# Optimization experiments

Measured on AMD Instinct MI355X. Metric: run time of the kernel, lower is better.

Reference implementation:

```python
import jax, jax.numpy as jnp
import numpy as np

BN_EPS = 1e-3  # Keras BatchNormalization default epsilon


def setup_inputs() -> dict:
    key = jax.random.key(0)
    ks = jax.random.split(key, 8)
    N, F, H, S, E = 30000, 16, 16, 8, 300000
    return {
        "x": jax.random.normal(ks[0], (N, F), dtype=jnp.float32),
        "e": jax.random.uniform(ks[1], (E, S), dtype=jnp.float32),
        "src": jax.random.randint(ks[2], (E,), 0, N),
        "dst": jax.random.randint(ks[3], (E,), 0, N),
        "Wk": jax.random.normal(ks[4], (S, F * H), dtype=jnp.float32) * 0.1,
        "bk": jnp.zeros((F * H,), dtype=jnp.float32),
        "Wr": jax.random.normal(ks[5], (F, H), dtype=jnp.float32) * 0.1,
        "br": jnp.zeros((H,), dtype=jnp.float32),
        "gamma": jnp.ones((H,), dtype=jnp.float32),
        "beta": jnp.zeros((H,), dtype=jnp.float32),
        "mmean": jnp.zeros((H,), dtype=jnp.float32),
        "mvar": jnp.ones((H,), dtype=jnp.float32),
        "Wd": jax.random.normal(ks[6], (H, 3), dtype=jnp.float32) * 0.1,
        "bd": jnp.zeros((3,), dtype=jnp.float32),
    }


def reference(x, e, src, dst, Wk, bk, Wr, br, gamma, beta, mmean, mvar, Wd, bd):
    N, F = x.shape
    H = Wr.shape[1]
    # ECCConv: per-edge filter generated from edge features -> [E, F, H]
    kernels = (e @ Wk + bk).reshape(e.shape[0], F, H)
    # message: gather source node feats, apply per-edge kernel
    msg = jnp.einsum('ef,efh->eh', x[src], kernels)  # [E, H]
    # scatter-sum aggregate to target nodes
    agg = jax.ops.segment_sum(msg, dst, num_segments=N)  # [N, H]
    h = jax.nn.relu(agg + x @ Wr + br)
    # BatchNormalization (inference: moving stats); Dropout = identity at eval
    h = (h - mmean) / jnp.sqrt(mvar + BN_EPS) * gamma + beta
    pooled = jnp.max(h, axis=0, keepdims=True)  # GlobalMaxPool, single mode -> [1, H]
    return pooled @ Wd + bd  # [1, 3]
```

## Files before the change

### kernel.cpp

```cpp
#include <hip/hip_runtime.h>

#define BN_EPS 1e-3f

typedef float vf4 __attribute__((ext_vector_type(4)));
typedef _Float16 half8 __attribute__((ext_vector_type(8)));

__device__ __forceinline__ unsigned int f2k(float f) {
    unsigned int u = __float_as_uint(f);
    return (u & 0x80000000u) ? ~u : (u | 0x80000000u);
}
__device__ __forceinline__ float k2f(unsigned int u) {
    return __uint_as_float((u & 0x80000000u) ? (u & 0x7FFFFFFFu) : ~u);
}

template <int S, int F, int H>
__global__ void node_pre(const float* __restrict__ x,
                         const float* __restrict__ Wk,
                         const float* __restrict__ bk,
                         const float* __restrict__ Wr,
                         const float* __restrict__ br,
                         _Float16* __restrict__ y2h,
                         float* __restrict__ agg,
                         unsigned int* __restrict__ pooled_u,
                         int N) {
    if (blockIdx.x == 0 && threadIdx.x < H) pooled_u[threadIdx.x] = 0u;

    int t = blockIdx.x * blockDim.x + threadIdx.x;
    int n = t / H;
    int h = t % H;
    if (n >= N) return;

    float xf[F];
#pragma unroll
    for (int f = 0; f < F; ++f) xf[f] = x[n * F + f];

    _Float16* yrow = y2h + (size_t)n * (S + 1) * H + h;
#pragma unroll
    for (int s = 0; s < S; ++s) {
        float acc = 0.f;
#pragma unroll
        for (int f = 0; f < F; ++f) acc += xf[f] * Wk[(s * F + f) * H + h];
        yrow[s * H] = (_Float16)acc;
    }

    float accb = 0.f, accr = 0.f;
#pragma unroll
    for (int f = 0; f < F; ++f) {
        accb += xf[f] * bk[f * H + h];
        accr += xf[f] * Wr[f * H + h];
    }
    yrow[S * H] = (_Float16)accb;
    agg[(size_t)n * H + h] = accr + br[h];
}

template <int S, int H>
__global__ void __launch_bounds__(256)
edge_scatter(const float* __restrict__ efeat,
             const int* __restrict__ src,
             const int* __restrict__ dst,
             const _Float16* __restrict__ y2h,
             float* __restrict__ agg,
             int E) {
    constexpr int EB = 256;
    constexpr int LDW = EB + 4;
    __shared__ float msg[H][LDW];
    __shared__ int sdst[EB];

    int t = threadIdx.x;
    int e0 = blockIdx.x * EB;

    int el = t >> 1;
    int hi = t & 1;
    int ell0 = el, ell1 = el + 128;
    int ec0 = min(e0 + ell0, E - 1);
    int ec1 = min(e0 + ell1, E - 1);

    int sn0 = __builtin_nontemporal_load(src + ec0);
    int sn1 = __builtin_nontemporal_load(src + ec1);
    if (hi == 0) {
        sdst[ell0] = __builtin_nontemporal_load(dst + ec0);
        sdst[ell1] = __builtin_nontemporal_load(dst + ec1);
    }

    const vf4* e40 = (const vf4*)(efeat + (size_t)ec0 * S);
    const vf4* e41 = (const vf4*)(efeat + (size_t)ec1 * S);
    vf4 ea0 = __builtin_nontemporal_load(e40);
    vf4 eb0 = __builtin_nontemporal_load(e40 + 1);
    vf4 ea1 = __builtin_nontemporal_load(e41);
    vf4 eb1 = __builtin_nontemporal_load(e41 + 1);
    float es0[S + 1] = {ea0.x, ea0.y, ea0.z, ea0.w, eb0.x, eb0.y, eb0.z, eb0.w, 1.0f};
    float es1[S + 1] = {ea1.x, ea1.y, ea1.z, ea1.w, eb1.x, eb1.y, eb1.z, eb1.w, 1.0f};

    const _Float16* yb0 = y2h + (size_t)sn0 * (S + 1) * H + hi * 8;
    const _Float16* yb1 = y2h + (size_t)sn1 * (S + 1) * H + hi * 8;

    float m0[8] = {0.f, 0.f, 0.f, 0.f, 0.f, 0.f, 0.f, 0.f};
    float m1[8] = {0.f, 0.f, 0.f, 0.f, 0.f, 0.f, 0.f, 0.f};
#pragma unroll
    for (int s = 0; s <= S; ++s) {
        half8 hv0 = *(const half8*)(yb0 + s * H);
        half8 hv1 = *(const half8*)(yb1 + s * H);
#pragma unroll
        for (int j = 0; j < 8; ++j) {
            m0[j] += es0[s] * (float)hv0[j];
            m1[j] += es1[s] * (float)hv1[j];
        }
    }
#pragma unroll
    for (int j = 0; j < 8; ++j) {
        msg[hi * 8 + j][ell0] = m0[j];
        msg[hi * 8 + j][ell1] = m1[j];
    }

    __syncthreads();

    int e2 = t >> 4;
    int h = t & 15;
#pragma unroll
    for (int p = 0; p < 16; ++p) {
        int el2 = p * 16 + e2;
        if (e0 + el2 < E) {
            unsafeAtomicAdd(&agg[(size_t)sdst[el2] * H + h], msg[h][el2]);
        }
    }
}

template <int H>
__global__ void bn_relu_max(const float* __restrict__ agg,
                            const float* __restrict__ gamma,
                            const float* __restrict__ beta,
                            const float* __restrict__ mmean,
                            const float* __restrict__ mvar,
                            unsigned int* __restrict__ pooled_u,
                            int N) {
    __shared__ unsigned int smax[H];
    if (threadIdx.x < H) smax[threadIdx.x] = 0u;
    __syncthreads();

    int t = blockIdx.x * blockDim.x + threadIdx.x;
    int stride = gridDim.x * blockDim.x;
    int h = t % H;

    float scale = gamma[h] * rsqrtf(mvar[h] + BN_EPS);
    float shift = beta[h] - mmean[h] * scale;

    float best = -INFINITY;
    int total = N * H;
    for (int i = t; i < total; i += stride) {
        float v = agg[i];
        v = v > 0.f ? v : 0.f;
        v = v * scale + shift;
        best = fmaxf(best, v);
    }
    atomicMax(&smax[h], f2k(best));
    __syncthreads();
    if (threadIdx.x < H) atomicMax(&pooled_u[threadIdx.x], smax[threadIdx.x]);
}

template <int H>
__global__ void final_matvec(const unsigned int* __restrict__ pooled_u,
                             const float* __restrict__ Wd,
                             const float* __restrict__ bd,
                             float* __restrict__ out,
                             int HOUT) {
    int j = threadIdx.x;
    if (j >= HOUT) return;
    float acc = bd[j];
#pragma unroll
    for (int hh = 0; hh < H; ++hh) acc += k2f(pooled_u[hh]) * Wd[hh * HOUT + j];
    out[j] = acc;
}

extern "C" void kernel_launch(void* const* d_in, const int* in_sizes, int n_in,
                              void* d_out, int out_size, void* d_ws, size_t ws_size,
                              hipStream_t stream) {
    const float* x     = (const float*)d_in[0];
    const float* e     = (const float*)d_in[1];
    const int*   src   = (const int*)d_in[2];
    const int*   dst   = (const int*)d_in[3];
    const float* Wk    = (const float*)d_in[4];
    const float* bk    = (const float*)d_in[5];
    const float* Wr    = (const float*)d_in[6];
    const float* br    = (const float*)d_in[7];
    const float* gamma = (const float*)d_in[8];
    const float* beta  = (const float*)d_in[9];
    const float* mmean = (const float*)d_in[10];
    const float* mvar  = (const float*)d_in[11];
    const float* Wd    = (const float*)d_in[12];
    const float* bd    = (const float*)d_in[13];

    constexpr int S = 8, F = 16, H = 16;
    const int E = in_sizes[2];
    const int N = in_sizes[0] / F;
    const int HOUT = in_sizes[13];

    _Float16* y2h = (_Float16*)d_ws;
    float* agg = (float*)(y2h + (size_t)N * (S + 1) * H);
    unsigned int* pooled_u = (unsigned int*)(agg + (size_t)N * H);

    const int T = 256;
    int nh = N * H;
    node_pre<S, F, H><<<(nh + T - 1) / T, T, 0, stream>>>(
        x, Wk, bk, Wr, br, y2h, agg, pooled_u, N);

    int eblocks = (E + 255) / 256;
    edge_scatter<S, H><<<eblocks, T, 0, stream>>>(
        e, src, dst, y2h, agg, E);

    bn_relu_max<H><<<1024, T, 0, stream>>>(agg, gamma, beta, mmean, mvar, pooled_u, N);

    final_matvec<H><<<1, 64, 0, stream>>>(pooled_u, Wd, bd, (float*)d_out, HOUT);
}
```

Before: 142.5 us.

## Fuse final matvec into BN-max kernel via last-block pattern, vectorize loads

Merges the final dense matvec into the BN/ReLU/max reduction kernel using an atomic completion counter, so the last block to finish computes the output. This removes one kernel launch. The reduction loop now reads agg as float4 and tracks four per-channel maxima per thread, and the grid shrinks from 1024 to 240 blocks. The counter slot is zeroed in node_pre, and the change adds threadfences and one global atomic per block.

```diff
diff --git a/kernel.cpp b/kernel.cpp
--- a/kernel.cpp
+++ b/kernel.cpp
@@ -23,7 +23,7 @@
                          float* __restrict__ agg,
                          unsigned int* __restrict__ pooled_u,
                          int N) {
-    if (blockIdx.x == 0 && threadIdx.x < H) pooled_u[threadIdx.x] = 0u;
+    if (blockIdx.x == 0 && threadIdx.x < H + 1) pooled_u[threadIdx.x] = 0u;
 
     int t = blockIdx.x * blockDim.x + threadIdx.x;
     int n = t / H;
@@ -126,49 +126,68 @@
 }
 
 template <int H>
-__global__ void bn_relu_max(const float* __restrict__ agg,
-                            const float* __restrict__ gamma,
-                            const float* __restrict__ beta,
-                            const float* __restrict__ mmean,
-                            const float* __restrict__ mvar,
-                            unsigned int* __restrict__ pooled_u,
-                            int N) {
+__global__ void __launch_bounds__(256)
+bn_relu_max_final(const float* __restrict__ agg,
+                  const float* __restrict__ gamma,
+                  const float* __restrict__ beta,
+                  const float* __restrict__ mmean,
+                  const float* __restrict__ mvar,
+                  unsigned int* __restrict__ pooled_u,
+                  const float* __restrict__ Wd,
+                  const float* __restrict__ bd,
+                  float* __restrict__ out,
+                  int N, int HOUT) {
     __shared__ unsigned int smax[H];
     if (threadIdx.x < H) smax[threadIdx.x] = 0u;
     __syncthreads();
 
     int t = blockIdx.x * blockDim.x + threadIdx.x;
     int stride = gridDim.x * blockDim.x;
-    int h = t % H;
-
-    float scale = gamma[h] * rsqrtf(mvar[h] + BN_EPS);
-    float shift = beta[h] - mmean[h] * scale;
-
-    float best = -INFINITY;
-    int total = N * H;
-    for (int i = t; i < total; i += stride) {
-        float v = agg[i];
-        v = v > 0.f ? v : 0.f;
-        v = v * scale + shift;
-        best = fmaxf(best, v);
-    }
-    atomicMax(&smax[h], f2k(best));
+    int h4 = (t & 3) * 4;
+
+    float sc[4], sh[4];
+#pragma unroll
+    for (int j = 0; j < 4; ++j) {
+        float s = gamma[h4 + j] * rsqrtf(mvar[h4 + j] + BN_EPS);
+        sc[j] = s;
+        sh[j] = beta[h4 + j] - mmean[h4 + j] * s;
+    }
+
+    float best[4] = {-INFINITY, -INFINITY, -INFINITY, -INFINITY};
+    int total4 = N * H / 4;
+    const vf4* agg4 = (const vf4*)agg;
+    for (int i = t; i < total4; i += stride) {
+        vf4 v = agg4[i];
+#pragma unroll
+        for (int j = 0; j < 4; ++j) {
+            float w = v[j] > 0.f ? v[j] : 0.f;
+            w = w * sc[j] + sh[j];
+            best[j] = fmaxf(best[j], w);
+        }
+    }
+#pragma unroll
+    for (int j = 0; j < 4; ++j) atomicMax(&smax[h4 + j], f2k(best[j]));
     __syncthreads();
     if (threadIdx.x < H) atomicMax(&pooled_u[threadIdx.x], smax[threadIdx.x]);
-}
-
-template <int H>
-__global__ void final_matvec(const unsigned int* __restrict__ pooled_u,
-                             const float* __restrict__ Wd,
-                             const float* __restrict__ bd,
-                             float* __restrict__ out,
-                             int HOUT) {
-    int j = threadIdx.x;
-    if (j >= HOUT) return;
-    float acc = bd[j];
-#pragma unroll
-    for (int hh = 0; hh < H; ++hh) acc += k2f(pooled_u[hh]) * Wd[hh * HOUT + j];
-    out[j] = acc;
+
+    __threadfence();
+    __shared__ bool is_last;
+    if (threadIdx.x == 0) {
+        unsigned int done = atomicAdd(&pooled_u[H], 1u);
+        is_last = (done == gridDim.x - 1);
+    }
+    __syncthreads();
+    if (is_last && threadIdx.x < HOUT) {
+        __threadfence();
+        int j = threadIdx.x;
+        float acc = bd[j];
+#pragma unroll
+        for (int hh = 0; hh < H; ++hh) {
+            unsigned int u = atomicOr(&pooled_u[hh], 0u);
+            acc += k2f(u) * Wd[hh * HOUT + j];
+        }
+        out[j] = acc;
+    }
 }
 
 extern "C" void kernel_launch(void* const* d_in, const int* in_sizes, int n_in,
@@ -207,7 +226,6 @@
     edge_scatter<S, H><<<eblocks, T, 0, stream>>>(
         e, src, dst, y2h, agg, E);
 
-    bn_relu_max<H><<<1024, T, 0, stream>>>(agg, gamma, beta, mmean, mvar, pooled_u, N);
-
-    final_matvec<H><<<1, 64, 0, stream>>>(pooled_u, Wd, bd, (float*)d_out, HOUT);
-}
+    bn_relu_max_final<H><<<240, T, 0, stream>>>(
+        agg, gamma, beta, mmean, mvar, pooled_u, Wd, bd, (float*)d_out, N, HOUT);
+}
```

Result: slower. 145.4 us (+2.1%).
